# Performance work log

Measured on AMD Instinct MI355X. Metric: run time of the kernel, lower is better.

Reference implementation:

```python
import jax, jax.numpy as jnp
import numpy as np
from jax.scipy.special import logsumexp


def _mixture_log_cdf(x, pi, mu, s):
    # x: [B,C,H,W]; pi,mu,s: [B,C,H,W,K]. log CDF of mixture of logistics.
    z = (x[..., None] - mu) * jnp.exp(-s)
    return logsumexp(jax.nn.log_softmax(pi, axis=-1) + jax.nn.log_sigmoid(z), axis=-1)


def _mixture_log_pdf(x, pi, mu, s):
    z = (x[..., None] - mu) * jnp.exp(-s)
    log_p = z - s - 2.0 * jax.nn.softplus(z)  # logistic log-density per component
    return logsumexp(jax.nn.log_softmax(pi, axis=-1) + log_p, axis=-1)


def setup_inputs() -> dict:
    key = jax.random.key(0)
    ks = jax.random.split(key, 8)
    B, C, H, W, K = 32, 8, 64, 64, 16
    shp = (B, C, H, W)
    mshp = (B, C, H, W, K)
    return {
        "x_change": jax.random.normal(ks[0], shp, jnp.float32),
        "x_id": jax.random.normal(ks[1], shp, jnp.float32),
        "sldj": jnp.zeros((B,), jnp.float32),
        "a": 0.1 * jax.random.normal(ks[2], shp, jnp.float32),
        "b": 0.1 * jax.random.normal(ks[3], shp, jnp.float32),
        "pi": jax.random.normal(ks[4], mshp, jnp.float32),
        "mu": jax.random.normal(ks[5], mshp, jnp.float32),
        "s": 0.1 * jax.random.normal(ks[6], mshp, jnp.float32),
    }


def reference(x_change, x_id, sldj, a, b, pi, mu, s):
    B = x_change.shape[0]
    # forward (reverse=False) Flow++ MixLogCDF coupling
    log_cdf = _mixture_log_cdf(x_change, pi, mu, s)  # [B,C,H,W], values <= 0
    u = jnp.exp(log_cdf)                             # CDF in (0,1)
    # sigmoid inverse (logit) with log-det: z = log(u) - log(1-u); ldj = -log(u) - log(1-u)
    out = log_cdf - jnp.log1p(-u)
    scale_ldj = -log_cdf - jnp.log1p(-u)
    out = (out + b) * jnp.exp(a)
    logistic_ldj = _mixture_log_pdf(x_change, pi, mu, s)
    sldj = sldj + jnp.sum((logistic_ldj + scale_ldj + a).reshape(B, -1), axis=-1)
    return out, x_id, sldj
```

## Files before the change

### kernel.cpp

```cpp
#include <hip/hip_runtime.h>
#include <math.h>

#define KCOMP 16
#define CHW 32768
#define LOG2E 1.44269504088896340736f
#define LN2   0.69314718055994530942f

__global__ void init_sldj_kernel(const float* __restrict__ sldj,
                                 float* __restrict__ out_sldj, int B) {
    int i = blockIdx.x * blockDim.x + threadIdx.x;
    if (i < B) out_sldj[i] = sldj[i];
}

__global__ __launch_bounds__(256) void coupling_kernel(
    const float* __restrict__ x_change, const float* __restrict__ x_id,
    const float* __restrict__ a, const float* __restrict__ b,
    const float* __restrict__ pi, const float* __restrict__ mu,
    const float* __restrict__ s, float* __restrict__ out, int N) {
    const int i = blockIdx.x * blockDim.x + threadIdx.x;
    float ldj_term = 0.0f;
    if (i < N) {
        const float x = x_change[i];
        const size_t base = (size_t)i * KCOMP;

        float p[KCOMP];
        {
            const float4* pv = (const float4*)(pi + base);
#pragma unroll
            for (int c = 0; c < 4; ++c) {
                float4 t0 = pv[c];
                p[4 * c + 0] = t0.x; p[4 * c + 1] = t0.y;
                p[4 * c + 2] = t0.z; p[4 * c + 3] = t0.w;
            }
        }
        float pmax = p[0];
#pragma unroll
        for (int k = 1; k < KCOMP; ++k) pmax = fmaxf(pmax, p[k]);

        float w[KCOMP];
        float psum = 0.0f;
#pragma unroll
        for (int k = 0; k < KCOMP; ++k) {
            w[k] = __builtin_amdgcn_exp2f((p[k] - pmax) * LOG2E);
            psum += w[k];
        }

        float m[KCOMP], sv[KCOMP];
        {
            const float4* mv = (const float4*)(mu + base);
            const float4* svv = (const float4*)(s + base);
#pragma unroll
            for (int c = 0; c < 4; ++c) {
                float4 t1 = mv[c];
                m[4 * c + 0] = t1.x; m[4 * c + 1] = t1.y;
                m[4 * c + 2] = t1.z; m[4 * c + 3] = t1.w;
                float4 t2 = svv[c];
                sv[4 * c + 0] = t2.x; sv[4 * c + 1] = t2.y;
                sv[4 * c + 2] = t2.z; sv[4 * c + 3] = t2.w;
            }
        }

        float cdf = 0.0f, omu = 0.0f, pdf = 0.0f;
#pragma unroll
        for (int k = 0; k < KCOMP; ++k) {
            const float ez = __builtin_amdgcn_exp2f(-sv[k] * LOG2E);
            const float z = (x - m[k]) * ez;
            const float enz = __builtin_amdgcn_exp2f(-z * LOG2E);
            const float g = __builtin_amdgcn_rcpf(1.0f + enz);
            const float wg = w[k] * g;
            cdf += wg;
            omu += wg * enz;
            pdf += w[k] * ez * g * g * enz;
        }

        const float l2psum = __builtin_amdgcn_logf(psum);
        const float l2cdf  = __builtin_amdgcn_logf(cdf);
        const float l2omu  = __builtin_amdgcn_logf(fmaxf(omu, 1e-38f));
        const float l2pdf  = __builtin_amdgcn_logf(fmaxf(pdf, 1e-38f));

        const float av = a[i];
        const float bv = b[i];
        const float outv = (l2cdf - l2omu) * LN2;
        out[i] = (outv + bv) * __builtin_amdgcn_exp2f(av * LOG2E);
        out[(size_t)N + i] = x_id[i];
        ldj_term = (l2pdf + l2psum - l2cdf - l2omu) * LN2 + av;
    }

    float v = ldj_term;
#pragma unroll
    for (int off = 32; off > 0; off >>= 1) v += __shfl_down(v, off);
    __shared__ float ws[4];
    const int wid = threadIdx.x >> 6;
    if ((threadIdx.x & 63) == 0) ws[wid] = v;
    __syncthreads();
    if (threadIdx.x == 0) {
        const float tot = ws[0] + ws[1] + ws[2] + ws[3];
        const int batch = (blockIdx.x * blockDim.x) / CHW;
        atomicAdd(out + 2 * (size_t)N + batch, tot);
    }
}

extern "C" void kernel_launch(void* const* d_in, const int* in_sizes, int n_in,
                              void* d_out, int out_size, void* d_ws, size_t ws_size,
                              hipStream_t stream) {
    const float* x_change = (const float*)d_in[0];
    const float* x_id     = (const float*)d_in[1];
    const float* sldj     = (const float*)d_in[2];
    const float* a        = (const float*)d_in[3];
    const float* b        = (const float*)d_in[4];
    const float* pi       = (const float*)d_in[5];
    const float* mu       = (const float*)d_in[6];
    const float* s        = (const float*)d_in[7];
    float* out = (float*)d_out;

    const int N = in_sizes[0];
    const int B = in_sizes[2];

    init_sldj_kernel<<<1, 64, 0, stream>>>(sldj, out + 2 * (size_t)N, B);

    const int block = 256;
    const int grid = (N + block - 1) / block;
    coupling_kernel<<<grid, block, 0, stream>>>(x_change, x_id, a, b, pi, mu, s, out, N);
}
```

Measured before the change: 222.7 us.

## Stage mixture params via direct global-to-LDS loads and split components across threads

Result: slower. 231.1 us (+3.8%).

```diff
diff --git a/kernel.cpp b/kernel.cpp
--- a/kernel.cpp
+++ b/kernel.cpp
@@ -1,10 +1,15 @@
 #include <hip/hip_runtime.h>
 #include <math.h>
 
-#define KCOMP 16
+#define NELEM 1048576
 #define CHW 32768
+#define TILE 256
+#define NBLK (NELEM / TILE)
 #define LOG2E 1.44269504088896340736f
 #define LN2   0.69314718055994530942f
+
+typedef const __attribute__((address_space(1))) void g_void;
+typedef __attribute__((address_space(3))) void l_void;
 
 __global__ void init_sldj_kernel(const float* __restrict__ sldj,
                                  float* __restrict__ out_sldj, int B) {
@@ -16,87 +21,100 @@
     const float* __restrict__ x_change, const float* __restrict__ x_id,
     const float* __restrict__ a, const float* __restrict__ b,
     const float* __restrict__ pi, const float* __restrict__ mu,
-    const float* __restrict__ s, float* __restrict__ out, int N) {
-    const int i = blockIdx.x * blockDim.x + threadIdx.x;
-    float ldj_term = 0.0f;
-    if (i < N) {
-        const float x = x_change[i];
-        const size_t base = (size_t)i * KCOMP;
+    const float* __restrict__ s, float* __restrict__ out) {
+    __shared__ __align__(16) float ldsP[TILE * 16];
+    __shared__ __align__(16) float ldsM[TILE * 16];
+    __shared__ __align__(16) float ldsS[TILE * 16];
 
-        float p[KCOMP];
-        {
-            const float4* pv = (const float4*)(pi + base);
+    const int t = threadIdx.x;
+    const int w = t >> 6;
+    const int l = t & 63;
+    const int e0 = blockIdx.x * TILE;
+
+    {
+        const size_t gbase = (size_t)e0 * 16 + (size_t)(w * 1024 + l * 4);
+        const int lbase = w * 1024 + l * 4;
 #pragma unroll
-            for (int c = 0; c < 4; ++c) {
-                float4 t0 = pv[c];
-                p[4 * c + 0] = t0.x; p[4 * c + 1] = t0.y;
-                p[4 * c + 2] = t0.z; p[4 * c + 3] = t0.w;
-            }
+        for (int c = 0; c < 4; ++c) {
+            __builtin_amdgcn_global_load_lds((g_void*)(pi + gbase + c * 256),
+                                             (l_void*)(ldsP + lbase + c * 256), 16, 0, 0);
+            __builtin_amdgcn_global_load_lds((g_void*)(mu + gbase + c * 256),
+                                             (l_void*)(ldsM + lbase + c * 256), 16, 0, 0);
+            __builtin_amdgcn_global_load_lds((g_void*)(s + gbase + c * 256),
+                                             (l_void*)(ldsS + lbase + c * 256), 16, 0, 0);
         }
-        float pmax = p[0];
+    }
+
+    const int kq = t & 3;
+    const int g = t >> 2;
+    float xv[4], av[4], bv[4];
 #pragma unroll
-        for (int k = 1; k < KCOMP; ++k) pmax = fmaxf(pmax, p[k]);
+    for (int p = 0; p < 4; ++p) {
+        const int e = e0 + p * 64 + g;
+        xv[p] = x_change[e];
+        av[p] = a[e];
+        bv[p] = b[e];
+    }
+    out[(size_t)NELEM + e0 + t] = x_id[e0 + t];
 
-        float w[KCOMP];
-        float psum = 0.0f;
+    __builtin_amdgcn_s_waitcnt(0);
+    __syncthreads();
+
+    float ldj = 0.0f;
+    const float4* P4 = (const float4*)ldsP;
+    const float4* M4 = (const float4*)ldsM;
+    const float4* S4 = (const float4*)ldsS;
 #pragma unroll
-        for (int k = 0; k < KCOMP; ++k) {
-            w[k] = __builtin_amdgcn_exp2f((p[k] - pmax) * LOG2E);
-            psum += w[k];
-        }
+    for (int p = 0; p < 4; ++p) {
+        const int idx = (p * 64 + g) * 4 + kq;
+        const float4 pv = P4[idx];
+        const float4 mv = M4[idx];
+        const float4 sv = S4[idx];
+        const float x = xv[p];
 
-        float m[KCOMP], sv[KCOMP];
-        {
-            const float4* mv = (const float4*)(mu + base);
-            const float4* svv = (const float4*)(s + base);
+        float psum = 0.0f, cdf = 0.0f, omu = 0.0f, pdf = 0.0f;
+        const float pk[4] = {pv.x, pv.y, pv.z, pv.w};
+        const float mk[4] = {mv.x, mv.y, mv.z, mv.w};
+        const float sk[4] = {sv.x, sv.y, sv.z, sv.w};
 #pragma unroll
-            for (int c = 0; c < 4; ++c) {
-                float4 t1 = mv[c];
-                m[4 * c + 0] = t1.x; m[4 * c + 1] = t1.y;
-                m[4 * c + 2] = t1.z; m[4 * c + 3] = t1.w;
-                float4 t2 = svv[c];
-                sv[4 * c + 0] = t2.x; sv[4 * c + 1] = t2.y;
-                sv[4 * c + 2] = t2.z; sv[4 * c + 3] = t2.w;
-            }
-        }
-
-        float cdf = 0.0f, omu = 0.0f, pdf = 0.0f;
-#pragma unroll
-        for (int k = 0; k < KCOMP; ++k) {
-            const float ez = __builtin_amdgcn_exp2f(-sv[k] * LOG2E);
-            const float z = (x - m[k]) * ez;
+        for (int j = 0; j < 4; ++j) {
+            const float wk = __builtin_amdgcn_exp2f(pk[j] * LOG2E);
+            const float ez = __builtin_amdgcn_exp2f(-sk[j] * LOG2E);
+            const float z = (x - mk[j]) * ez;
             const float enz = __builtin_amdgcn_exp2f(-z * LOG2E);
-            const float g = __builtin_amdgcn_rcpf(1.0f + enz);
-            const float wg = w[k] * g;
+            const float gg = __builtin_amdgcn_rcpf(1.0f + enz);
+            const float wg = wk * gg;
+            psum += wk;
             cdf += wg;
             omu += wg * enz;
-            pdf += w[k] * ez * g * g * enz;
+            pdf += wk * ez * gg * gg * enz;
         }
+        psum += __shfl_xor(psum, 1); psum += __shfl_xor(psum, 2);
+        cdf  += __shfl_xor(cdf, 1);  cdf  += __shfl_xor(cdf, 2);
+        omu  += __shfl_xor(omu, 1);  omu  += __shfl_xor(omu, 2);
+        pdf  += __shfl_xor(pdf, 1);  pdf  += __shfl_xor(pdf, 2);
 
-        const float l2psum = __builtin_amdgcn_logf(psum);
-        const float l2cdf  = __builtin_amdgcn_logf(cdf);
-        const float l2omu  = __builtin_amdgcn_logf(fmaxf(omu, 1e-38f));
-        const float l2pdf  = __builtin_amdgcn_logf(fmaxf(pdf, 1e-38f));
-
-        const float av = a[i];
-        const float bv = b[i];
-        const float outv = (l2cdf - l2omu) * LN2;
-        out[i] = (outv + bv) * __builtin_amdgcn_exp2f(av * LOG2E);
-        out[(size_t)N + i] = x_id[i];
-        ldj_term = (l2pdf + l2psum - l2cdf - l2omu) * LN2 + av;
+        if (kq == 0) {
+            const float l2psum = __builtin_amdgcn_logf(psum);
+            const float l2cdf  = __builtin_amdgcn_logf(cdf);
+            const float l2omu  = __builtin_amdgcn_logf(fmaxf(omu, 1e-38f));
+            const float l2pdf  = __builtin_amdgcn_logf(fmaxf(pdf, 1e-38f));
+            const float outv = (l2cdf - l2omu) * LN2;
+            out[e0 + p * 64 + g] = (outv + bv[p]) * __builtin_amdgcn_exp2f(av[p] * LOG2E);
+            ldj += (l2pdf + l2psum - l2cdf - l2omu) * LN2 + av[p];
+        }
     }
 
-    float v = ldj_term;
+    float v = ldj;
 #pragma unroll
     for (int off = 32; off > 0; off >>= 1) v += __shfl_down(v, off);
     __shared__ float ws[4];
-    const int wid = threadIdx.x >> 6;
-    if ((threadIdx.x & 63) == 0) ws[wid] = v;
+    if ((t & 63) == 0) ws[w] = v;
     __syncthreads();
-    if (threadIdx.x == 0) {
+    if (t == 0) {
         const float tot = ws[0] + ws[1] + ws[2] + ws[3];
-        const int batch = (blockIdx.x * blockDim.x) / CHW;
-        atomicAdd(out + 2 * (size_t)N + batch, tot);
+        const int batch = blockIdx.x >> 7;
+        atomicAdd(out + 2 * (size_t)NELEM + batch, tot);
     }
 }
 
@@ -113,12 +131,8 @@
     const float* s        = (const float*)d_in[7];
     float* out = (float*)d_out;
 
-    const int N = in_sizes[0];
     const int B = in_sizes[2];
 
-    init_sldj_kernel<<<1, 64, 0, stream>>>(sldj, out + 2 * (size_t)N, B);
-
-    const int block = 256;
-    const int grid = (N + block - 1) / block;
-    coupling_kernel<<<grid, block, 0, stream>>>(x_change, x_id, a, b, pi, mu, s, out, N);
+    init_sldj_kernel<<<1, 64, 0, stream>>>(sldj, out + 2 * (size_t)NELEM, B);
+    coupling_kernel<<<NBLK, 256, 0, stream>>>(x_change, x_id, a, b, pi, mu, s, out);
 }
```
